# Optimization experiments

Measured on AMD Instinct MI355X. Metric: run time of the kernel, lower is better.

Reference implementation:

```python
import jax, jax.numpy as jnp
import numpy as np

N, IN_DIM, OUT_DIM, HEADS = 50000, 128, 32, 8
E = 800000
F = OUT_DIM * HEADS  # 256 fused output features
SEM_HID = 128        # SemanticAttention hidden size (HAN default)


def setup_inputs() -> dict:
    key = jax.random.key(0)
    ks = jax.random.split(key, 16)
    inp = {
        "h": jax.random.normal(ks[0], (N, IN_DIM), jnp.float32),
        "src_a": jax.random.randint(ks[1], (E,), 0, N, jnp.int32),
        "dst_a": jax.random.randint(ks[2], (E,), 0, N, jnp.int32),
        "src_b": jax.random.randint(ks[3], (E,), 0, N, jnp.int32),
        "dst_b": jax.random.randint(ks[4], (E,), 0, N, jnp.int32),
    }
    s = 1.0 / np.sqrt(IN_DIM)
    # per-metapath GATConv params
    inp["W_a"] = jax.random.normal(ks[5], (IN_DIM, F), jnp.float32) * s
    inp["al_a"] = jax.random.normal(ks[6], (HEADS, OUT_DIM), jnp.float32) * 0.1
    inp["ar_a"] = jax.random.normal(ks[7], (HEADS, OUT_DIM), jnp.float32) * 0.1
    inp["bias_a"] = jnp.zeros((F,), jnp.float32)
    inp["W_b"] = jax.random.normal(ks[8], (IN_DIM, F), jnp.float32) * s
    inp["al_b"] = jax.random.normal(ks[9], (HEADS, OUT_DIM), jnp.float32) * 0.1
    inp["ar_b"] = jax.random.normal(ks[10], (HEADS, OUT_DIM), jnp.float32) * 0.1
    inp["bias_b"] = jnp.zeros((F,), jnp.float32)
    # semantic attention params
    inp["Wsem"] = jax.random.normal(ks[11], (F, SEM_HID), jnp.float32) / np.sqrt(F)
    inp["bsem"] = jnp.zeros((SEM_HID,), jnp.float32)
    inp["wsem"] = jax.random.normal(ks[12], (SEM_HID,), jnp.float32) / np.sqrt(SEM_HID)
    return inp


def gat_conv(h, src, dst, W, al, ar, bias):
    # h: [N, in_dim] -> feat: [N, H, D]
    feat = (h @ W).reshape(N, HEADS, OUT_DIM)
    el = (feat * al).sum(-1)  # [N, H]
    er = (feat * ar).sum(-1)  # [N, H]
    e = jax.nn.leaky_relu(el[src] + er[dst], 0.2)  # [E, H]
    # edge softmax over incoming edges of each dst node (numerically stable)
    m = jax.ops.segment_max(e, dst, num_segments=N)        # -inf for empty
    ex = jnp.exp(e - m[dst])                               # [E, H]
    denom = jax.ops.segment_sum(ex, dst, num_segments=N)   # [N, H]
    msg = feat[src] * ex[:, :, None]                       # [E, H, D]
    out = jax.ops.segment_sum(msg, dst, num_segments=N)    # [N, H, D]
    out = out / jnp.where(denom > 0, denom, 1.0)[:, :, None]
    return jax.nn.elu(out.reshape(N, F) + bias)


def reference(h, src_a, dst_a, src_b, dst_b,
              W_a, al_a, ar_a, bias_a,
              W_b, al_b, ar_b, bias_b,
              Wsem, bsem, wsem):
    z_a = gat_conv(h, src_a, dst_a, W_a, al_a, ar_a, bias_a)
    z_b = gat_conv(h, src_b, dst_b, W_b, al_b, ar_b, bias_b)
    z = jnp.stack([z_a, z_b], axis=1)                 # [N, M, F]
    q = jnp.tanh(z @ Wsem + bsem) @ wsem              # [N, M]
    beta = jax.nn.softmax(q.mean(axis=0))             # [M]
    return (z * beta[None, :, None]).sum(axis=1)      # [N, F]
```

## Files before the change

kernel.cpp:

```cpp
#include <hip/hip_runtime.h>
#include <stdint.h>

#define NN 50000
#define EE 800000
#define IN_DIM 128
#define OUT_DIM 32
#define HEADS 8
#define FF 256
#define SH 128
#define NPAD 50048
#define FEXT 272
#define CAP 64
#define CSTRIDE 16

#define GEMM_BLKS 782
#define FILL_G   6250
#define PULL_G   12500

#define P_BTA0   128
#define P_BTB0   (P_BTA0 + FEXT)
#define P_G      (P_BTB0 + FEXT)

#define F_GEMM   (2 * GEMM_BLKS)
#define F_G      (F_GEMM + FILL_G)

#define C_G      (2 * PULL_G)
#define D_G      (2 * GEMM_BLKS)

#define QSLOTS   16

typedef short s16x8 __attribute__((ext_vector_type(8)));
typedef float f32x4 __attribute__((ext_vector_type(4)));
typedef float f32x2 __attribute__((ext_vector_type(2)));

__device__ __forceinline__ float b2f(unsigned short u) {
    union { unsigned int i; float f; } v; v.i = ((unsigned int)u) << 16; return v.f;
}
__device__ __forceinline__ unsigned short f2b(float f) {
    union { float f; unsigned int i; } v; v.f = f;
    unsigned int i = v.i;
    unsigned int r = (i + 0x7FFFu + ((i >> 16) & 1u)) >> 16;
    return (unsigned short)r;
}

__device__ __forceinline__ void buildBT_one(
    const float* __restrict__ W, const float* __restrict__ al,
    const float* __restrict__ ar, unsigned short* __restrict__ BT,
    int fp, int k)
{
    float v;
    if (fp < FF) {
        v = W[(size_t)k * FF + fp];
    } else if (fp < FF + 8) {
        int hh = fp - FF;
        float s = 0.f;
        #pragma unroll
        for (int d = 0; d < 32; ++d) s += W[(size_t)k * FF + hh * 32 + d] * al[hh * 32 + d];
        v = s;
    } else {
        int hh = fp - FF - 8;
        float s = 0.f;
        #pragma unroll
        for (int d = 0; d < 32; ++d) s += W[(size_t)k * FF + hh * 32 + d] * ar[hh * 32 + d];
        v = s;
    }
    BT[(size_t)fp * IN_DIM + k] = f2b(v);
}

__device__ __forceinline__ void dev_fill(
    int idx, const int* __restrict__ src, const int* __restrict__ dst,
    int* __restrict__ counts, unsigned short* __restrict__ perm)
{
    int d = dst[idx];
    int r = atomicAdd(&counts[d * CSTRIDE], 1);
    if (r < CAP) perm[d * CAP + r] = (unsigned short)src[idx];
}

__device__ __forceinline__ void dev_gemm(
    int gb, int t, const float* __restrict__ h,
    const unsigned short* __restrict__ BT,
    unsigned short* __restrict__ feat,
    float* __restrict__ el, float* __restrict__ er)
{
    int wave = t >> 6, lane = t & 63;
    int quad = lane >> 4, l16 = lane & 15;
    int nbase = gb * 64 + wave * 16;
    int n = nbase + l16;
    int nr = (n < NN) ? n : (NN - 1);
    const float* hrow = h + (size_t)nr * IN_DIM + quad * 8;
    s16x8 nfr[4];
    #pragma unroll
    for (int kt = 0; kt < 4; ++kt) {
        float4 p0 = *(const float4*)(hrow + kt * 32);
        float4 p1 = *(const float4*)(hrow + kt * 32 + 4);
        s16x8 v;
        v[0] = (short)f2b(p0.x); v[1] = (short)f2b(p0.y);
        v[2] = (short)f2b(p0.z); v[3] = (short)f2b(p0.w);
        v[4] = (short)f2b(p1.x); v[5] = (short)f2b(p1.y);
        v[6] = (short)f2b(p1.z); v[7] = (short)f2b(p1.w);
        nfr[kt] = v;
    }
    bool live = (n < NN);
    #pragma unroll 1
    for (int ft = 0; ft < 17; ++ft) {
        const unsigned short* brow = BT + (size_t)(ft * 16 + l16) * IN_DIM + quad * 8;
        f32x4 c = {0.f, 0.f, 0.f, 0.f};
        #pragma unroll
        for (int kt = 0; kt < 4; ++kt) {
            s16x8 ffr = *(const s16x8*)(brow + kt * 32);
            c = __builtin_amdgcn_mfma_f32_16x16x32_bf16(ffr, nfr[kt], c, 0, 0, 0);
        }
        if (ft < 16) {
            if (live) {
                ushort4 r;
                r.x = f2b(c[0]); r.y = f2b(c[1]); r.z = f2b(c[2]); r.w = f2b(c[3]);
                *(ushort4*)(feat + (size_t)n * FF + ft * 16 + quad * 4) = r;
            }
        } else if (live) {
            #pragma unroll
            for (int r = 0; r < 4; ++r) {
                int jp = quad * 4 + r;
                if (jp < 8) el[n * HEADS + jp] = c[r];
                else        er[n * HEADS + (jp - 8)] = c[r];
            }
        }
    }
}

__device__ __forceinline__ void dev_pull(
    int blk, int tid,
    const int* __restrict__ counts, const unsigned short* __restrict__ perm,
    const float* __restrict__ el, const float* __restrict__ er,
    const unsigned short* __restrict__ feat, const float* __restrict__ bias,
    unsigned short* __restrict__ zb)
{
    int wave = tid >> 6;
    int lane = tid & 63;
    int n = blk * 4 + wave;
    int sub = lane >> 5;
    int l32 = lane & 31;
    int head = l32 >> 2;
    int fbase = l32 * 8;
    int deg = counts[n * CSTRIDE];
    if (deg > CAP) deg = CAP;
    int base = n * CAP;
    float ern = er[n * HEADS + head];
    float den = 0.f;
    f32x2 acc2[4];
    #pragma unroll
    for (int u = 0; u < 4; ++u) { acc2[u][0] = 0.f; acc2[u][1] = 0.f; }

#define PROC(EV, FV) {                                               \
        float x = (EV) + ern;                                        \
        x = fmaxf(x, 0.2f * x);                                      \
        float ex = __expf(x);                                        \
        den += ex;                                                   \
        f32x2 ex2; ex2[0] = ex; ex2[1] = ex;                         \
        const unsigned int* fp = (const unsigned int*)&(FV);         \
        _Pragma("unroll")                                            \
        for (int u = 0; u < 4; ++u) {                                \
            union { unsigned int i; float f; } lo, hi;               \
            lo.i = fp[u] << 16; hi.i = fp[u] & 0xFFFF0000u;          \
            f32x2 v; v[0] = lo.f; v[1] = hi.f;                       \
            acc2[u] += v * ex2;                                      \
        } }

    int jp = sub;
    #pragma unroll 1
    for (; jp + 6 < deg; jp += 8) {
        int s0 = perm[base + jp];
        int s1 = perm[base + jp + 2];
        int s2 = perm[base + jp + 4];
        int s3 = perm[base + jp + 6];
        float e0 = el[s0 * HEADS + head];
        float e1 = el[s1 * HEADS + head];
        float e2 = el[s2 * HEADS + head];
        float e3 = el[s3 * HEADS + head];
        uint4 f0 = *(const uint4*)(feat + (size_t)s0 * FF + fbase);
        uint4 f1 = *(const uint4*)(feat + (size_t)s1 * FF + fbase);
        uint4 f2 = *(const uint4*)(feat + (size_t)s2 * FF + fbase);
        uint4 f3 = *(const uint4*)(feat + (size_t)s3 * FF + fbase);
        PROC(e0, f0); PROC(e1, f1); PROC(e2, f2); PROC(e3, f3);
    }
    #pragma unroll 1
    for (; jp + 2 < deg; jp += 4) {
        int s0 = perm[base + jp];
        int s1 = perm[base + jp + 2];
        float e0 = el[s0 * HEADS + head];
        float e1 = el[s1 * HEADS + head];
        uint4 f0 = *(const uint4*)(feat + (size_t)s0 * FF + fbase);
        uint4 f1 = *(const uint4*)(feat + (size_t)s1 * FF + fbase);
        PROC(e0, f0); PROC(e1, f1);
    }
    if (jp < deg) {
        int s0 = perm[base + jp];
        float e0 = el[s0 * HEADS + head];
        uint4 f0 = *(const uint4*)(feat + (size_t)s0 * FF + fbase);
        PROC(e0, f0);
    }
#undef PROC

    float accf[8];
    #pragma unroll
    for (int u = 0; u < 4; ++u) {
        accf[2 * u]     = acc2[u][0];
        accf[2 * u + 1] = acc2[u][1];
    }

    den += __shfl_xor(den, 32, 64);
    #pragma unroll
    for (int u = 0; u < 8; ++u) accf[u] += __shfl_xor(accf[u], 32, 64);

    if (den <= 0.f) den = 1.f;
    float inv = 1.f / den;
    float4 b0 = *(const float4*)(bias + fbase);
    float4 b1 = *(const float4*)(bias + fbase + 4);
    float bv[8] = {b0.x, b0.y, b0.z, b0.w, b1.x, b1.y, b1.z, b1.w};
    if (sub == 0) {
        ushort4 r0, r1;
        unsigned short rr[8];
        #pragma unroll
        for (int u = 0; u < 8; ++u) {
            float ov = accf[u] * inv + bv[u];
            ov = (ov > 0.f) ? ov : (__expf(ov) - 1.f);
            rr[u] = f2b(ov);
        }
        r0.x = rr[0]; r0.y = rr[1]; r0.z = rr[2]; r0.w = rr[3];
        r1.x = rr[4]; r1.y = rr[5]; r1.z = rr[6]; r1.w = rr[7];
        *(ushort4*)(zb + (size_t)n * FF + fbase) = r0;
        *(ushort4*)(zb + (size_t)n * FF + fbase + 4) = r1;
    }
}

__global__ __launch_bounds__(256) void prep(
    const float* __restrict__ Wsem, unsigned short* __restrict__ WsemT,
    const float* __restrict__ W_a, const float* __restrict__ al_a,
    const float* __restrict__ ar_a, unsigned short* __restrict__ BT_a,
    const float* __restrict__ W_b, const float* __restrict__ al_b,
    const float* __restrict__ ar_b, unsigned short* __restrict__ BT_b)
{
    int b = blockIdx.x, t = threadIdx.x;
    if (b < P_BTA0) {
        WsemT[b * FF + t] = f2b(Wsem[(size_t)t * SH + b]);
    } else if (b < P_BTB0) {
        if (t < IN_DIM) buildBT_one(W_a, al_a, ar_a, BT_a, b - P_BTA0, t);
    } else {
        if (t < IN_DIM) buildBT_one(W_b, al_b, ar_b, BT_b, b - P_BTB0, t);
    }
}

__global__ __launch_bounds__(256) void megaF(
    const float* __restrict__ h,
    const unsigned short* __restrict__ BT_a, const unsigned short* __restrict__ BT_b,
    unsigned short* __restrict__ feat_a, unsigned short* __restrict__ feat_b,
    float* __restrict__ el_a, float* __restrict__ er_a,
    float* __restrict__ el_b, float* __restrict__ er_b,
    const int* __restrict__ src_a, const int* __restrict__ dst_a,
    const int* __restrict__ src_b, const int* __restrict__ dst_b,
    int* __restrict__ counts_a, int* __restrict__ counts_b,
    unsigned short* __restrict__ perm_a, unsigned short* __restrict__ perm_b)
{
    int b = blockIdx.x, t = threadIdx.x;
    if (b >= F_GEMM) {
        int idx = (b - F_GEMM) * 256 + t;
        if (idx < EE) dev_fill(idx, src_a, dst_a, counts_a, perm_a);
        else          dev_fill(idx - EE, src_b, dst_b, counts_b, perm_b);
        return;
    }
    int mp = (b >= GEMM_BLKS);
    int gb = mp ? b - GEMM_BLKS : b;
    dev_gemm(gb, t, h,
             mp ? BT_b : BT_a, mp ? feat_b : feat_a,
             mp ? el_b : el_a, mp ? er_b : er_a);
}

__global__ __launch_bounds__(256, 8) void megaC(
    const int* __restrict__ counts_a, const int* __restrict__ counts_b,
    const unsigned short* __restrict__ perm_a, const unsigned short* __restrict__ perm_b,
    const float* __restrict__ el_a, const float* __restrict__ er_a,
    const float* __restrict__ el_b, const float* __restrict__ er_b,
    const unsigned short* __restrict__ feat_a, const unsigned short* __restrict__ feat_b,
    const float* __restrict__ bias_a, const float* __restrict__ bias_b,
    unsigned short* __restrict__ zb_a, unsigned short* __restrict__ zb_b)
{
    int bb = blockIdx.x;
    int mp = (bb >= PULL_G);
    int blk = mp ? bb - PULL_G : bb;
    dev_pull(blk, threadIdx.x,
             mp ? counts_b : counts_a, mp ? perm_b : perm_a,
             mp ? el_b : el_a, mp ? er_b : er_a,
             mp ? feat_b : feat_a, mp ? bias_b : bias_a,
             mp ? zb_b : zb_a);
}

__global__ __launch_bounds__(256) void megaD(
    const unsigned short* __restrict__ zb_a, const unsigned short* __restrict__ zb_b,
    const unsigned short* __restrict__ WsemT,
    const float* __restrict__ bsem, const float* __restrict__ wsem,
    float* __restrict__ qsumP)
{
    int bb = blockIdx.x;
    int mp = (bb >= GEMM_BLKS);
    int blk = mp ? bb - GEMM_BLKS : bb;
    const unsigned short* zb = mp ? zb_b : zb_a;

    int wave = threadIdx.x >> 6, lane = threadIdx.x & 63;
    int quad = lane >> 4, l16 = lane & 15;
    int nbase = blk * 64 + wave * 16;
    const unsigned short* arow = zb + (size_t)(nbase + l16) * FF + quad * 8;
    s16x8 afr[8];
    #pragma unroll
    for (int kt = 0; kt < 8; ++kt)
        afr[kt] = *(const s16x8*)(arow + kt * 32);
    float qacc = 0.f;
    #pragma unroll 1
    for (int jt = 0; jt < 8; ++jt) {
        int jj = jt * 16 + l16;
        const unsigned short* brow = WsemT + (size_t)jj * FF + quad * 8;
        f32x4 c = {0.f, 0.f, 0.f, 0.f};
        #pragma unroll
        for (int kt = 0; kt < 8; ++kt) {
            s16x8 bfr = *(const s16x8*)(brow + kt * 32);
            c = __builtin_amdgcn_mfma_f32_16x16x32_bf16(afr[kt], bfr, c, 0, 0, 0);
        }
        float bj = bsem[jj], wj = wsem[jj];
        #pragma unroll
        for (int r = 0; r < 4; ++r) {
            int n = nbase + quad * 4 + r;
            float y = c[r] + bj;
            y = fminf(fmaxf(y, -10.f), 10.f);
            float t = __expf(2.f * y);
            float tv = (t - 1.f) * __builtin_amdgcn_rcpf(t + 1.f) * wj;
            qacc += (n < NN) ? tv : 0.f;
        }
    }
    #pragma unroll
    for (int o = 1; o < 64; o <<= 1) qacc += __shfl_xor(qacc, o, 64);
    if (lane == 0)
        atomicAdd(&qsumP[(mp * QSLOTS + (blk & (QSLOTS - 1))) * 16], qacc);
}

__global__ __launch_bounds__(256) void combine_kernel(
    const unsigned short* __restrict__ za,
    const unsigned short* __restrict__ zbm,
    float* __restrict__ out, const float* __restrict__ qsumP)
{
    size_t i = (size_t)blockIdx.x * blockDim.x + threadIdx.x;
    size_t base = i * 8;
    if (base >= (size_t)NN * FF) return;
    float qa = 0.f, qb = 0.f;
    #pragma unroll
    for (int s = 0; s < QSLOTS; ++s) {
        qa += qsumP[s * 16];
        qb += qsumP[(QSLOTS + s) * 16];
    }
    qa *= (1.f / NN); qb *= (1.f / NN);
    float mx = fmaxf(qa, qb);
    float ea = __expf(qa - mx), eb = __expf(qb - mx);
    float inv = 1.f / (ea + eb);
    float b0 = ea * inv, b1 = eb * inv;
    uint4 va = *(const uint4*)(za + base);
    uint4 vb = *(const uint4*)(zbm + base);
    const unsigned short* pa = (const unsigned short*)&va;
    const unsigned short* pb = (const unsigned short*)&vb;
    float4 r0, r1;
    r0.x = b0 * b2f(pa[0]) + b1 * b2f(pb[0]);
    r0.y = b0 * b2f(pa[1]) + b1 * b2f(pb[1]);
    r0.z = b0 * b2f(pa[2]) + b1 * b2f(pb[2]);
    r0.w = b0 * b2f(pa[3]) + b1 * b2f(pb[3]);
    r1.x = b0 * b2f(pa[4]) + b1 * b2f(pb[4]);
    r1.y = b0 * b2f(pa[5]) + b1 * b2f(pb[5]);
    r1.z = b0 * b2f(pa[6]) + b1 * b2f(pb[6]);
    r1.w = b0 * b2f(pa[7]) + b1 * b2f(pb[7]);
    *(float4*)(out + base) = r0;
    *(float4*)(out + base + 4) = r1;
}

extern "C" void kernel_launch(void* const* d_in, const int* in_sizes, int n_in,
                              void* d_out, int out_size, void* d_ws, size_t ws_size,
                              hipStream_t stream)
{
    const float* h      = (const float*)d_in[0];
    const int* src_a    = (const int*)d_in[1];
    const int* dst_a    = (const int*)d_in[2];
    const int* src_b    = (const int*)d_in[3];
    const int* dst_b    = (const int*)d_in[4];
    const float* W_a    = (const float*)d_in[5];
    const float* al_a   = (const float*)d_in[6];
    const float* ar_a   = (const float*)d_in[7];
    const float* bias_a = (const float*)d_in[8];
    const float* W_b    = (const float*)d_in[9];
    const float* al_b   = (const float*)d_in[10];
    const float* ar_b   = (const float*)d_in[11];
    const float* bias_b = (const float*)d_in[12];
    const float* Wsem   = (const float*)d_in[13];
    const float* bsem   = (const float*)d_in[14];
    const float* wsem   = (const float*)d_in[15];
    float* out = (float*)d_out;

    char* ws = (char*)d_ws;
    size_t o = 0;
    auto alloc = [&](size_t bytes) -> char* {
        char* p = ws + o;
        o += (bytes + 255) & ~(size_t)255;
        return p;
    };
    unsigned short* BT_a   = (unsigned short*)alloc((size_t)FEXT * IN_DIM * 2);
    unsigned short* BT_b   = (unsigned short*)alloc((size_t)FEXT * IN_DIM * 2);
    unsigned short* feat_a = (unsigned short*)alloc((size_t)NN * FF * 2);
    unsigned short* feat_b = (unsigned short*)alloc((size_t)NN * FF * 2);
    unsigned short* zb_a   = (unsigned short*)alloc((size_t)NPAD * FF * 2);
    unsigned short* zb_b   = (unsigned short*)alloc((size_t)NPAD * FF * 2);
    unsigned short* WsemT  = (unsigned short*)alloc((size_t)SH * FF * 2);
    float* el_a    = (float*)alloc((size_t)NN * HEADS * 4);
    float* er_a    = (float*)alloc((size_t)NN * HEADS * 4);
    float* el_b    = (float*)alloc((size_t)NN * HEADS * 4);
    float* er_b    = (float*)alloc((size_t)NN * HEADS * 4);
    unsigned short* perm_a = (unsigned short*)alloc((size_t)NN * CAP * 2);
    unsigned short* perm_b = (unsigned short*)alloc((size_t)NN * CAP * 2);
    char* zspan0   = ws + o;
    int* counts_a  = (int*)alloc((size_t)NN * CSTRIDE * 4);
    int* counts_b  = (int*)alloc((size_t)NN * CSTRIDE * 4);
    float* qsumP   = (float*)alloc((size_t)2 * QSLOTS * 16 * 4);
    size_t zspan   = (size_t)((ws + o) - zspan0);

    hipMemsetAsync(zspan0, 0, zspan, stream);
    prep<<<P_G, 256, 0, stream>>>(Wsem, WsemT,
                                  W_a, al_a, ar_a, BT_a,
                                  W_b, al_b, ar_b, BT_b);
    megaF<<<F_G, 256, 0, stream>>>(h, BT_a, BT_b, feat_a, feat_b,
                                   el_a, er_a, el_b, er_b,
                                   src_a, dst_a, src_b, dst_b,
                                   counts_a, counts_b, perm_a, perm_b);
    megaC<<<C_G, 256, 0, stream>>>(counts_a, counts_b, perm_a, perm_b,
                                   el_a, er_a, el_b, er_b,
                                   feat_a, feat_b, bias_a, bias_b, zb_a, zb_b);
    megaD<<<D_G, 256, 0, stream>>>(zb_a, zb_b, WsemT, bsem, wsem, qsumP);
    combine_kernel<<<(int)(((size_t)NN * FF / 8 + 255) / 256), 256, 0, stream>>>(zb_a, zb_b, out, qsumP);
}
```

Before: 424.5 us.

## Fuse semantic-attention scoring into the aggregation kernel using shared-memory rows

The separate semantic-attention kernel is removed. Each aggregation block now writes its 4 finished node rows to shared memory and immediately runs the Wsem MFMA projection, tanh and wsem dot on them. This avoids re-reading the full bf16 z arrays from global memory and saves one kernel launch. In exchange, every one of the many small blocks re-reads the whole WsemT matrix from cache, wastes 3/4 of each MFMA tile by replicating 4 rows to fill 16, and issues many more contended atomics into the q accumulators.

New measurement: 494.3 us. 1.16x slower.

```diff
diff --git a/kernel.cpp b/kernel.cpp
--- a/kernel.cpp
+++ b/kernel.cpp
@@ -25,7 +25,6 @@
 #define F_G      (F_GEMM + FILL_G)
 
 #define C_G      (2 * PULL_G)
-#define D_G      (2 * GEMM_BLKS)
 
 #define QSLOTS   16
 
@@ -132,7 +131,7 @@
     const int* __restrict__ counts, const unsigned short* __restrict__ perm,
     const float* __restrict__ el, const float* __restrict__ er,
     const unsigned short* __restrict__ feat, const float* __restrict__ bias,
-    unsigned short* __restrict__ zb)
+    unsigned short* __restrict__ zb, unsigned short* __restrict__ zrow)
 {
     int wave = tid >> 6;
     int lane = tid & 63;
@@ -229,6 +228,8 @@
         r1.x = rr[4]; r1.y = rr[5]; r1.z = rr[6]; r1.w = rr[7];
         *(ushort4*)(zb + (size_t)n * FF + fbase) = r0;
         *(ushort4*)(zb + (size_t)n * FF + fbase + 4) = r1;
+        *(ushort4*)(zrow + fbase) = r0;
+        *(ushort4*)(zrow + fbase + 4) = r1;
     }
 }
 
@@ -281,62 +282,60 @@
     const float* __restrict__ el_b, const float* __restrict__ er_b,
     const unsigned short* __restrict__ feat_a, const unsigned short* __restrict__ feat_b,
     const float* __restrict__ bias_a, const float* __restrict__ bias_b,
-    unsigned short* __restrict__ zb_a, unsigned short* __restrict__ zb_b)
-{
+    unsigned short* __restrict__ zb_a, unsigned short* __restrict__ zb_b,
+    const unsigned short* __restrict__ WsemT,
+    const float* __restrict__ bsem, const float* __restrict__ wsem,
+    float* __restrict__ qsumP)
+{
+    __shared__ __align__(16) unsigned short zlds[4][256];
     int bb = blockIdx.x;
     int mp = (bb >= PULL_G);
     int blk = mp ? bb - PULL_G : bb;
+
     dev_pull(blk, threadIdx.x,
              mp ? counts_b : counts_a, mp ? perm_b : perm_a,
              mp ? el_b : el_a, mp ? er_b : er_a,
              mp ? feat_b : feat_a, mp ? bias_b : bias_a,
-             mp ? zb_b : zb_a);
-}
-
-__global__ __launch_bounds__(256) void megaD(
-    const unsigned short* __restrict__ zb_a, const unsigned short* __restrict__ zb_b,
-    const unsigned short* __restrict__ WsemT,
-    const float* __restrict__ bsem, const float* __restrict__ wsem,
-    float* __restrict__ qsumP)
-{
-    int bb = blockIdx.x;
-    int mp = (bb >= GEMM_BLKS);
-    int blk = mp ? bb - GEMM_BLKS : bb;
-    const unsigned short* zb = mp ? zb_b : zb_a;
+             mp ? zb_b : zb_a, zlds[threadIdx.x >> 6]);
+
+    __syncthreads();
 
     int wave = threadIdx.x >> 6, lane = threadIdx.x & 63;
     int quad = lane >> 4, l16 = lane & 15;
-    int nbase = blk * 64 + wave * 16;
-    const unsigned short* arow = zb + (size_t)(nbase + l16) * FF + quad * 8;
-    s16x8 afr[8];
-    #pragma unroll
-    for (int kt = 0; kt < 8; ++kt)
-        afr[kt] = *(const s16x8*)(arow + kt * 32);
+    const unsigned short* zsrc = zlds[l16 & 3];
     float qacc = 0.f;
     #pragma unroll 1
-    for (int jt = 0; jt < 8; ++jt) {
+    for (int ji = 0; ji < 2; ++ji) {
+        int jt = wave * 2 + ji;
         int jj = jt * 16 + l16;
         const unsigned short* brow = WsemT + (size_t)jj * FF + quad * 8;
-        f32x4 c = {0.f, 0.f, 0.f, 0.f};
-        #pragma unroll
-        for (int kt = 0; kt < 8; ++kt) {
-            s16x8 bfr = *(const s16x8*)(brow + kt * 32);
-            c = __builtin_amdgcn_mfma_f32_16x16x32_bf16(afr[kt], bfr, c, 0, 0, 0);
+        f32x4 cA = {0.f, 0.f, 0.f, 0.f};
+        f32x4 cB = {0.f, 0.f, 0.f, 0.f};
+        #pragma unroll 1
+        for (int kt = 0; kt < 8; kt += 2) {
+            s16x8 a0 = *(const s16x8*)(zsrc + kt * 32 + quad * 8);
+            s16x8 a1 = *(const s16x8*)(zsrc + (kt + 1) * 32 + quad * 8);
+            s16x8 b0 = *(const s16x8*)(brow + kt * 32);
+            s16x8 b1 = *(const s16x8*)(brow + (kt + 1) * 32);
+            cA = __builtin_amdgcn_mfma_f32_16x16x32_bf16(a0, b0, cA, 0, 0, 0);
+            cB = __builtin_amdgcn_mfma_f32_16x16x32_bf16(a1, b1, cB, 0, 0, 0);
         }
         float bj = bsem[jj], wj = wsem[jj];
-        #pragma unroll
-        for (int r = 0; r < 4; ++r) {
-            int n = nbase + quad * 4 + r;
-            float y = c[r] + bj;
-            y = fminf(fmaxf(y, -10.f), 10.f);
-            float t = __expf(2.f * y);
-            float tv = (t - 1.f) * __builtin_amdgcn_rcpf(t + 1.f) * wj;
-            qacc += (n < NN) ? tv : 0.f;
+        if (quad == 0) {
+            #pragma unroll
+            for (int r = 0; r < 4; ++r) {
+                float y = cA[r] + cB[r] + bj;
+                y = fminf(fmaxf(y, -10.f), 10.f);
+                float t = __expf(2.f * y);
+                qacc += (t - 1.f) * __builtin_amdgcn_rcpf(t + 1.f) * wj;
+            }
         }
     }
-    #pragma unroll
-    for (int o = 1; o < 64; o <<= 1) qacc += __shfl_xor(qacc, o, 64);
-    if (lane == 0)
+    qacc += __shfl_xor(qacc, 1, 64);
+    qacc += __shfl_xor(qacc, 2, 64);
+    qacc += __shfl_xor(qacc, 4, 64);
+    qacc += __shfl_xor(qacc, 8, 64);
+    if ((lane & 15) == 0 && quad == 0)
         atomicAdd(&qsumP[(mp * QSLOTS + (blk & (QSLOTS - 1))) * 16], qacc);
 }
 
@@ -434,7 +433,7 @@
                                    counts_a, counts_b, perm_a, perm_b);
     megaC<<<C_G, 256, 0, stream>>>(counts_a, counts_b, perm_a, perm_b,
                                    el_a, er_a, el_b, er_b,
-                                   feat_a, feat_b, bias_a, bias_b, zb_a, zb_b);
-    megaD<<<D_G, 256, 0, stream>>>(zb_a, zb_b, WsemT, bsem, wsem, qsumP);
+                                   feat_a, feat_b, bias_a, bias_b, zb_a, zb_b,
+                                   WsemT, bsem, wsem, qsumP);
     combine_kernel<<<(int)(((size_t)NN * FF / 8 + 255) / 256), 256, 0, stream>>>(zb_a, zb_b, out, qsumP);
 }
```
